# Optimization experiments

Measured on AMD Instinct MI355X. Metric: run time of the kernel, lower is better.

Reference implementation:

```python
import jax, jax.numpy as jnp
import numpy as np
from jax import lax

NK, NV, DK, DV, K, C = 16, 32, 128, 128, 4, 2048
KEY_DIM = NK * DK
VAL_DIM = NV * DV
CONV_DIM = 2 * KEY_DIM + VAL_DIM
EPS = 1e-6


def setup_inputs() -> dict:
    key = jax.random.key(0)
    ks = jax.random.split(key, 10)
    B, T = 2, 2048
    s = 0.02
    return {
        "x": jax.random.normal(ks[0], (B, T, C), jnp.float32),
        "input_pos": jnp.arange(T, dtype=jnp.int32),
        "W_qkv": jax.random.normal(ks[1], (CONV_DIM, C), jnp.float32) * s,
        "W_z": jax.random.normal(ks[2], (VAL_DIM, C), jnp.float32) * s,
        "W_b": jax.random.normal(ks[3], (NV, C), jnp.float32) * s,
        "W_a": jax.random.normal(ks[4], (NV, C), jnp.float32) * s,
        "conv_w": jax.random.normal(ks[5], (CONV_DIM, 1, K), jnp.float32) * 0.1,
        "dt_bias": jnp.ones((NV,), jnp.float32),
        "A_log": jnp.log(jax.random.uniform(ks[6], (NV,), jnp.float32, 1e-3, 16.0)),
        "norm_w": jnp.ones((DV,), jnp.float32),
        "W_out": jax.random.normal(ks[7], (C, VAL_DIM), jnp.float32) * s,
        "conv_state": jnp.zeros((B, CONV_DIM, K), jnp.float32),
        "recurrent_state": jnp.zeros((B, NV, DK, DV), jnp.float32),
    }


def reference(x, input_pos, W_qkv, W_z, W_b, W_a, conv_w, dt_bias, A_log,
              norm_w, W_out, conv_state, recurrent_state):
    B, T, _ = x.shape
    # reset cached state when starting a new sequence (input_pos[0] == 0)
    keep = 1.0 - (input_pos[0] == 0).astype(x.dtype)
    conv_state = conv_state * keep
    state0 = recurrent_state * keep

    qkv = jnp.einsum('btc,dc->btd', x, W_qkv)                      # [B,T,CONV_DIM]
    z = jnp.einsum('btc,dc->btd', x, W_z).reshape(B, T, NV, DV)
    beta = jax.nn.sigmoid(jnp.einsum('btc,hc->bth', x, W_b))       # [B,T,NV]
    a = jnp.einsum('btc,hc->bth', x, W_a)
    g = -jnp.exp(A_log) * jax.nn.softplus(a + dt_bias)             # [B,T,NV]

    # causal depthwise conv using cached conv_state as left context
    conv_in = jnp.concatenate([conv_state, qkv.transpose(0, 2, 1)], axis=-1)  # [B,D,K+T]
    conv_out = lax.conv_general_dilated(
        conv_in, conv_w, (1,), 'VALID',
        dimension_numbers=('NCH', 'OIH', 'NCH'),
        feature_group_count=CONV_DIM)
    qkv_c = jax.nn.silu(conv_out[:, :, -T:]).transpose(0, 2, 1)    # [B,T,CONV_DIM]

    q = qkv_c[..., :KEY_DIM].reshape(B, T, NK, DK)
    k = qkv_c[..., KEY_DIM:2 * KEY_DIM].reshape(B, T, NK, DK)
    v = qkv_c[..., 2 * KEY_DIM:].reshape(B, T, NV, DV)
    q = q / jnp.maximum(jnp.linalg.norm(q, axis=-1, keepdims=True), 1e-12)
    k = k / jnp.maximum(jnp.linalg.norm(k, axis=-1, keepdims=True), 1e-12)
    rep = NV // NK
    if rep > 1:
        q = jnp.repeat(q, rep, axis=2)
        k = jnp.repeat(k, rep, axis=2)

    # gated delta-rule recurrence over time
    def step(carry, xs):
        q_i, k_i, v_i, g_i, b_i = xs                               # [B,H,*]
        new = (jnp.exp(g_i)[..., None, None] * carry
               + b_i[..., None, None] * (k_i[..., :, None] * v_i[..., None, :]))
        out = jnp.einsum('bhk,bhkv->bhv', q_i, new)
        return new, out

    xs = (q.transpose(1, 0, 2, 3), k.transpose(1, 0, 2, 3),
          v.transpose(1, 0, 2, 3), g.transpose(1, 0, 2), beta.transpose(1, 0, 2))
    state, outs = lax.scan(step, state0, xs)
    o = outs.transpose(1, 0, 2, 3)                                 # [B,T,NV,DV]

    # gated RMSNorm (Mamba2-style): gate with silu(z), then RMS-normalize
    o = o * jax.nn.silu(z)
    var = jnp.mean(o * o, axis=-1, keepdims=True)
    o = o * lax.rsqrt(var + EPS) * norm_w
    return jnp.einsum('btd,cd->btc', o.reshape(B, T, VAL_DIM), W_out)
```

## Files before the change

kernel.cpp:

```cpp
#include <hip/hip_runtime.h>
#include <hip/hip_bf16.h>
#include <math.h>

#define NKH 16
#define NVH 32
#define DKD 128
#define DVD 128
#define CDIM 2048
#define KEY_DIM 2048
#define VAL_DIM 4096
#define CONV_DIM 8192
#define BB 2
#define TT 2048
#define MROWS 4096
#define CH 64
#define NCHUNK 32

typedef unsigned short u16;
typedef __bf16 bf16x8 __attribute__((ext_vector_type(8)));
typedef float f32x4 __attribute__((ext_vector_type(4)));

__device__ __forceinline__ u16 f2bf(float f) {
    union { float f; unsigned u; } a; a.f = f;
    unsigned u = a.u;
    u += 0x7fffu + ((u >> 16) & 1u);
    return (u16)(u >> 16);
}
__device__ __forceinline__ float bf2f(u16 h) {
    union { unsigned u; float f; } a; a.u = ((unsigned)h) << 16;
    return a.f;
}
union BF8 { bf16x8 v; uint2 u2[2]; uint4 u4; u16 s[8]; };
__device__ __forceinline__ bf16x8 lds_ld8(const u16* p) {
    BF8 t; t.u2[0] = *(const uint2*)p; t.u2[1] = *(const uint2*)(p + 4); return t.v;
}
__device__ __forceinline__ bf16x8 lds_ld16(const u16* p) {
    BF8 t; t.u4 = *(const uint4*)p; return t.v;
}
__device__ __forceinline__ void lds_st8(u16* p, uint4 v) {
    *(uint2*)p = make_uint2(v.x, v.y); *(uint2*)(p + 4) = make_uint2(v.z, v.w);
}

__global__ __launch_bounds__(256) void fill_kernel(float* __restrict__ p, float v, int n) {
    int i = blockIdx.x * 256 + threadIdx.x;
    if (i < n) p[i] = v;
}

__global__ __launch_bounds__(256) void cast_kernel(const float* __restrict__ src,
                                                   u16* __restrict__ dst, int n4) {
    int i = blockIdx.x * 256 + threadIdx.x;
    if (i >= n4) return;
    float4 v = ((const float4*)src)[i];
    ushort4 r;
    r.x = f2bf(v.x); r.y = f2bf(v.y); r.z = f2bf(v.z); r.w = f2bf(v.w);
    ((ushort4*)dst)[i] = r;
}

template<int OUT_BF16>
__global__ __launch_bounds__(256) void gemm_nt(const u16* __restrict__ A,
                                               const u16* __restrict__ Bm,
                                               void* __restrict__ Cv,
                                               int M, int N, int K) {
    __shared__ __align__(16) u16 As[128 * 64];
    __shared__ __align__(16) u16 Bs[128 * 64];
    const int tid  = threadIdx.x;
    const int lane = tid & 63;
    const int wave = tid >> 6;
    const int m0 = blockIdx.y * 128;
    const int n0 = blockIdx.x * 128;
    const int wm = (wave & 1) * 64;
    const int wn = (wave >> 1) * 64;
    const int l15  = lane & 15;
    const int quad = lane >> 4;

    f32x4 acc[4][4];
#pragma unroll
    for (int i = 0; i < 4; ++i)
#pragma unroll
        for (int j = 0; j < 4; ++j) acc[i][j] = (f32x4)0.0f;

    const int crow = tid >> 3;
    const int ccol = (tid & 7) * 8;

    for (int k0 = 0; k0 < K; k0 += 64) {
#pragma unroll
        for (int p = 0; p < 4; ++p) {
            int row = p * 32 + crow;
            const u16* ga = A + (size_t)(m0 + row) * K + k0 + ccol;
            char* la = (char*)As + (size_t)(p * 256 + (wave << 6)) * 16;
            __builtin_amdgcn_global_load_lds((const __attribute__((address_space(1))) void*)ga,
                                             (__attribute__((address_space(3))) void*)la, 16, 0, 0);
            const u16* gb = Bm + (size_t)(n0 + row) * K + k0 + ccol;
            char* lb = (char*)Bs + (size_t)(p * 256 + (wave << 6)) * 16;
            __builtin_amdgcn_global_load_lds((const __attribute__((address_space(1))) void*)gb,
                                             (__attribute__((address_space(3))) void*)lb, 16, 0, 0);
        }
        __syncthreads();
#pragma unroll
        for (int kk = 0; kk < 64; kk += 32) {
            bf16x8 af[4], bfr[4];
#pragma unroll
            for (int i = 0; i < 4; ++i) {
                af[i]  = *(const bf16x8*)&As[(wm + i * 16 + l15) * 64 + kk + quad * 8];
                bfr[i] = *(const bf16x8*)&Bs[(wn + i * 16 + l15) * 64 + kk + quad * 8];
            }
#pragma unroll
            for (int i = 0; i < 4; ++i)
#pragma unroll
                for (int j = 0; j < 4; ++j)
                    acc[i][j] = __builtin_amdgcn_mfma_f32_16x16x32_bf16(af[i], bfr[j], acc[i][j], 0, 0, 0);
        }
        __syncthreads();
    }
#pragma unroll
    for (int i = 0; i < 4; ++i) {
#pragma unroll
        for (int j = 0; j < 4; ++j) {
#pragma unroll
            for (int r = 0; r < 4; ++r) {
                int grow = m0 + wm + i * 16 + quad * 4 + r;
                int gcol = n0 + wn + j * 16 + l15;
                if (OUT_BF16) {
                    ((u16*)Cv)[(size_t)grow * N + gcol] = f2bf(acc[i][j][r]);
                } else {
                    ((float*)Cv)[(size_t)grow * N + gcol] = acc[i][j][r];
                }
            }
        }
    }
}

template<int OUT_BF16>
__global__ __launch_bounds__(512, 2) void gemm_nt_256(const u16* __restrict__ A,
                                                      const u16* __restrict__ Bm,
                                                      void* __restrict__ Cv,
                                                      int M, int N, int K) {
    __shared__ __align__(16) u16 sA[2][256 * 64];
    __shared__ __align__(16) u16 sB[2][256 * 64];
    const int tid  = threadIdx.x;
    const int lane = tid & 63;
    const int wave = tid >> 6;
    const int wr   = wave >> 2;
    const int wc   = wave & 3;
    const int l15  = lane & 15;
    const int quad = lane >> 4;
    const int m0 = blockIdx.y * 256;
    const int n0 = blockIdx.x * 256;

    f32x4 acc[8][4];
#pragma unroll
    for (int i = 0; i < 8; ++i)
#pragma unroll
        for (int j = 0; j < 4; ++j) acc[i][j] = (f32x4)0.0f;

    auto stage = [&](int buf, int kk0) {
#pragma unroll
        for (int p = 0; p < 4; ++p) {
            const int gbase = p * 512 + wave * 64;
            const int g   = gbase + lane;
            const int row = g >> 3;
            const int sc  = (g & 7) ^ (row & 7);
            const u16* ga = A + (size_t)(m0 + row) * K + kk0 + sc * 8;
            __builtin_amdgcn_global_load_lds(
                (const __attribute__((address_space(1))) void*)ga,
                (__attribute__((address_space(3))) void*)((char*)&sA[buf][0] + (size_t)gbase * 16),
                16, 0, 0);
            const u16* gb = Bm + (size_t)(n0 + row) * K + kk0 + sc * 8;
            __builtin_amdgcn_global_load_lds(
                (const __attribute__((address_space(1))) void*)gb,
                (__attribute__((address_space(3))) void*)((char*)&sB[buf][0] + (size_t)gbase * 16),
                16, 0, 0);
        }
    };

    const int NT = K >> 6;
    stage(0, 0);

    for (int T = 0; T < NT; ++T) {
        const int P = T & 1;
        __builtin_amdgcn_sched_barrier(0);
        if (T + 1 < NT) {
            stage(P ^ 1, (T + 1) << 6);
            asm volatile("s_waitcnt vmcnt(8)" ::: "memory");
        } else {
            asm volatile("s_waitcnt vmcnt(0)" ::: "memory");
        }
        __builtin_amdgcn_s_barrier();
        __builtin_amdgcn_sched_barrier(0);
#pragma unroll
        for (int kk = 0; kk < 2; ++kk) {
            bf16x8 af[8], bfv[4];
#pragma unroll
            for (int i = 0; i < 8; ++i) {
                int row = wr * 128 + i * 16 + l15;
                int slot = ((kk * 4 + quad) ^ (l15 & 7)) * 8;
                af[i] = lds_ld16(&sA[P][row * 64 + slot]);
            }
#pragma unroll
            for (int j = 0; j < 4; ++j) {
                int row = wc * 64 + j * 16 + l15;
                int slot = ((kk * 4 + quad) ^ (l15 & 7)) * 8;
                bfv[j] = lds_ld16(&sB[P][row * 64 + slot]);
            }
#pragma unroll
            for (int i = 0; i < 8; ++i)
#pragma unroll
                for (int j = 0; j < 4; ++j)
                    acc[i][j] = __builtin_amdgcn_mfma_f32_16x16x32_bf16(af[i], bfv[j], acc[i][j], 0, 0, 0);
        }
        __builtin_amdgcn_sched_barrier(0);
        __builtin_amdgcn_s_barrier();
    }

#pragma unroll
    for (int i = 0; i < 8; ++i) {
#pragma unroll
        for (int j = 0; j < 4; ++j) {
#pragma unroll
            for (int r = 0; r < 4; ++r) {
                int grow = m0 + wr * 128 + i * 16 + quad * 4 + r;
                int gcol = n0 + wc * 64 + j * 16 + l15;
                if (OUT_BF16) {
                    ((u16*)Cv)[(size_t)grow * N + gcol] = f2bf(acc[i][j][r]);
                } else {
                    ((float*)Cv)[(size_t)grow * N + gcol] = acc[i][j][r];
                }
            }
        }
    }
}

__global__ __launch_bounds__(256) void bg_epilogue(const float* __restrict__ scores,
                                                   const float* __restrict__ dt_bias,
                                                   const float* __restrict__ A_log,
                                                   float* __restrict__ beta,
                                                   float* __restrict__ g) {
    int i = blockIdx.x * 256 + threadIdx.x;
    int row = i >> 6, col = i & 63;
    float s = scores[(size_t)row * 128 + col];
    if (col < 32) {
        beta[(size_t)row * 32 + col] = 1.f / (1.f + __expf(-s));
    } else {
        int h = col - 32;
        float aa = s + dt_bias[h];
        float sp = (aa > 20.f) ? aa : log1pf(__expf(aa));
        g[(size_t)row * 32 + h] = -__expf(A_log[h]) * sp;
    }
}

__global__ __launch_bounds__(256) void conv_silu_kernel(const u16* __restrict__ qkv,
                                                        const float* __restrict__ conv_w,
                                                        const float* __restrict__ conv_state,
                                                        const int* __restrict__ input_pos,
                                                        u16* __restrict__ qkvc) {
    const int d   = blockIdx.x * 256 + threadIdx.x;
    const int row = blockIdx.y;
    const int t   = row & (TT - 1);
    const int b   = row >> 11;
    const float keep = (input_pos[0] == 0) ? 0.f : 1.f;
    float4 w = *(const float4*)&conv_w[(size_t)d * 4];
    float acc = 0.f;
#pragma unroll
    for (int j = 0; j < 4; ++j) {
        int u = t + j - 3;
        float v;
        if (u >= 0) v = bf2f(qkv[(size_t)(b * TT + u) * CONV_DIM + d]);
        else        v = keep * conv_state[((size_t)b * CONV_DIM + d) * 4 + (u + 4)];
        acc += (&w.x)[j] * v;
    }
    float s = acc / (1.f + __expf(-acc));
    qkvc[(size_t)row * CONV_DIM + d] = f2bf(s);
}

__global__ __launch_bounds__(256) void qknorm_kernel(u16* __restrict__ qkvc) {
    const int gid  = blockIdx.x * 4 + (threadIdx.x >> 6);
    const int lane = threadIdx.x & 63;
    const int row  = gid >> 5;
    const int h    = gid & 31;
    u16* p = qkvc + (size_t)row * CONV_DIM + h * 128;
    ushort2 vb = *(ushort2*)&p[lane * 2];
    float v0 = bf2f(vb.x), v1 = bf2f(vb.y);
    float ss = v0 * v0 + v1 * v1;
#pragma unroll
    for (int off = 32; off; off >>= 1) ss += __shfl_xor(ss, off);
    float scale = 1.f / fmaxf(sqrtf(ss), 1e-12f);
    ushort2 r;
    r.x = f2bf(v0 * scale);
    r.y = f2bf(v1 * scale);
    *(ushort2*)&p[lane * 2] = r;
}

__global__ __launch_bounds__(64) void gates_kernel(const float* __restrict__ g,
                                                   const float* __restrict__ beta_,
                                                   float* __restrict__ gcum,
                                                   float* __restrict__ qsb,
                                                   float* __restrict__ wkb,
                                                   float* __restrict__ dLb) {
    const int bh = blockIdx.x, c = blockIdx.y;
    const int b = bh >> 5, h = bh & 31;
    const int t = threadIdx.x;
    const int row = b * TT + c * CH + t;
    float G = g[(size_t)row * 32 + h];
#pragma unroll
    for (int off = 1; off < 64; off <<= 1) {
        float x = __shfl_up(G, off);
        if (t >= off) G += x;
    }
    float GL = __shfl(G, 63);
    int oidx = bh * TT + c * CH + t;
    gcum[oidx] = G;
    qsb[oidx] = __expf(G);
    wkb[oidx] = __expf(GL - G) * beta_[(size_t)row * 32 + h];
    if (t == 0) dLb[bh * NCHUNK + c] = __expf(GL);
}

__global__ __launch_bounds__(256) void ktrans_kernel(const u16* __restrict__ qkvc,
                                                     u16* __restrict__ kT) {
    const int id = blockIdx.x;
    const int tt = id & 31, dkh = (id >> 5) & 1, hk = (id >> 6) & 15, b = id >> 10;
    const int t0 = tt * 64, dk0 = dkh * 64;
    __shared__ __align__(16) u16 tile[64 * 68];
#pragma unroll
    for (int it = 0; it < 2; ++it) {
        int idx = it * 256 + threadIdx.x;
        int tl = idx >> 3, c8 = (idx & 7) * 8;
        uint4 v = *(const uint4*)&qkvc[(size_t)(b * TT + t0 + tl) * CONV_DIM + KEY_DIM + hk * 128 + dk0 + c8];
        lds_st8(&tile[tl * 68 + c8], v);
    }
    __syncthreads();
#pragma unroll
    for (int it = 0; it < 2; ++it) {
        int idx = it * 256 + threadIdx.x;
        int dkl = idx >> 3, t8 = (idx & 7) * 8;
        unsigned w[4];
#pragma unroll
        for (int p = 0; p < 4; ++p) {
            unsigned lo = tile[(t8 + 2 * p) * 68 + dkl];
            unsigned hi = tile[(t8 + 2 * p + 1) * 68 + dkl];
            w[p] = lo | (hi << 16);
        }
        *(uint4*)&kT[((size_t)((b * 16 + hk) * 128 + dk0 + dkl)) * TT + t0 + t8] =
            make_uint4(w[0], w[1], w[2], w[3]);
    }
}

__global__ __launch_bounds__(256) void chunk_state_kernel(const u16* __restrict__ qkvc,
                                                          const u16* __restrict__ kT,
                                                          const float* __restrict__ qsb,
                                                          const float* __restrict__ wkb,
                                                          const float* __restrict__ dLb,
                                                          const float* __restrict__ rec_state,
                                                          const int* __restrict__ input_pos,
                                                          u16* __restrict__ o) {
    const int b = blockIdx.x, h = blockIdx.y, dvs = blockIdx.z;
    const int tid = threadIdx.x, lane = tid & 63, wave = tid >> 6;
    const int l15 = lane & 15, quad = lane >> 4;
    const int hq = h >> 1, bh = b * 32 + h;
    const float keep = (input_pos[0] == 0) ? 0.f : 1.f;

    __shared__ __align__(16) u16 sQ[64 * 132];
    __shared__ __align__(16) u16 sKT[128 * 68];
    __shared__ __align__(16) u16 sR[32 * 132];
    __shared__ float sQS[64];

    f32x4 st[2][2];
#pragma unroll
    for (int i = 0; i < 2; ++i)
#pragma unroll
        for (int j = 0; j < 2; ++j)
#pragma unroll
            for (int r = 0; r < 4; ++r) {
                int dv = dvs * 32 + i * 16 + quad * 4 + r;
                int dk = wave * 32 + j * 16 + l15;
                st[i][j][r] = keep * rec_state[((size_t)(bh * 128 + dk)) * 128 + dv];
            }

    for (int c = 0; c < NCHUNK; ++c) {
        const int t0 = c * CH;
#pragma unroll
        for (int i = 0; i < 2; ++i)
#pragma unroll
            for (int j = 0; j < 2; ++j)
#pragma unroll
                for (int r = 0; r < 4; ++r)
                    sR[(i * 16 + quad * 4 + r) * 132 + wave * 32 + j * 16 + l15] = f2bf(st[i][j][r]);
#pragma unroll
        for (int it = 0; it < 4; ++it) {
            int idx = it * 256 + tid;
            int t = idx >> 4, c8 = (idx & 15) * 8;
            uint4 v = *(const uint4*)&qkvc[(size_t)(b * TT + t0 + t) * CONV_DIM + hq * 128 + c8];
            lds_st8(&sQ[t * 132 + c8], v);
        }
        if (tid < 64) sQS[tid] = qsb[bh * TT + t0 + tid];
        __syncthreads();
        {
            f32x4 ao[2] = {(f32x4)0.0f, (f32x4)0.0f};
#pragma unroll
            for (int kk = 0; kk < 4; ++kk) {
                bf16x8 af = lds_ld8(&sQ[(wave * 16 + l15) * 132 + kk * 32 + quad * 8]);
                bf16x8 b0 = lds_ld8(&sR[(l15) * 132 + kk * 32 + quad * 8]);
                bf16x8 b1 = lds_ld8(&sR[(16 + l15) * 132 + kk * 32 + quad * 8]);
                ao[0] = __builtin_amdgcn_mfma_f32_16x16x32_bf16(af, b0, ao[0], 0, 0, 0);
                ao[1] = __builtin_amdgcn_mfma_f32_16x16x32_bf16(af, b1, ao[1], 0, 0, 0);
            }
#pragma unroll
            for (int j = 0; j < 2; ++j)
#pragma unroll
                for (int r = 0; r < 4; ++r) {
                    int t = wave * 16 + quad * 4 + r;
                    int dv = dvs * 32 + j * 16 + l15;
                    o[((size_t)(b * TT + t0 + t) * 32 + h) * 128 + dv] = f2bf(ao[j][r] * sQS[t]);
                }
        }
        __syncthreads();
#pragma unroll
        for (int it = 0; it < 4; ++it) {
            int idx = it * 256 + tid;
            int dk = idx >> 3, t8 = (idx & 7) * 8;
            uint4 v = *(const uint4*)&kT[((size_t)((b * 16 + hq) * 128 + dk)) * TT + t0 + t8];
            lds_st8(&sKT[dk * 68 + t8], v);
        }
        {
            int t = tid >> 2, dvo = (tid & 3) * 8;
            float w = wkb[bh * TT + t0 + t];
            BF8 v;
            v.u4 = *(const uint4*)&qkvc[(size_t)(b * TT + t0 + t) * CONV_DIM + 2 * KEY_DIM + h * 128 + dvs * 32 + dvo];
#pragma unroll
            for (int u = 0; u < 8; ++u)
                sR[(dvo + u) * 68 + t] = f2bf(bf2f(v.s[u]) * w);
        }
        __syncthreads();
        {
            float d = dLb[bh * NCHUNK + c];
#pragma unroll
            for (int i = 0; i < 2; ++i)
#pragma unroll
                for (int j = 0; j < 2; ++j)
#pragma unroll
                    for (int r = 0; r < 4; ++r) st[i][j][r] *= d;
#pragma unroll
            for (int kk = 0; kk < 2; ++kk) {
                bf16x8 af[2], bfv[2];
#pragma unroll
                for (int i = 0; i < 2; ++i)
                    af[i] = lds_ld8(&sR[(i * 16 + l15) * 68 + kk * 32 + quad * 8]);
#pragma unroll
                for (int j = 0; j < 2; ++j)
                    bfv[j] = lds_ld8(&sKT[(wave * 32 + j * 16 + l15) * 68 + kk * 32 + quad * 8]);
#pragma unroll
                for (int i = 0; i < 2; ++i)
#pragma unroll
                    for (int j = 0; j < 2; ++j)
                        st[i][j] = __builtin_amdgcn_mfma_f32_16x16x32_bf16(af[i], bfv[j], st[i][j], 0, 0, 0);
            }
        }
        __syncthreads();
    }
}

__global__ __launch_bounds__(256) void chunk_intra_kernel(const u16* __restrict__ qkvc,
                                                          const float* __restrict__ gcum,
                                                          const float* __restrict__ beta_,
                                                          u16* __restrict__ o) {
    const int b = blockIdx.x, h = blockIdx.y, c = blockIdx.z;
    const int tid = threadIdx.x, lane = tid & 63, wave = tid >> 6;
    const int l15 = lane & 15, quad = lane >> 4;
    const int hq = h >> 1, bh = b * 32 + h;
    const int t0 = c * CH;

    __shared__ __align__(16) u16 sQ[64 * 132];
    __shared__ __align__(16) u16 sK[64 * 132];
    __shared__ __align__(16) u16 sVT[128 * 68];
    __shared__ float sG[64];
    __shared__ float sB[64];

#pragma unroll
    for (int it = 0; it < 4; ++it) {
        int idx = it * 256 + tid;
        int t = idx >> 4, c8 = (idx & 15) * 8;
        size_t rbase = (size_t)(b * TT + t0 + t) * CONV_DIM;
        lds_st8(&sQ[t * 132 + c8], *(const uint4*)&qkvc[rbase + hq * 128 + c8]);
        lds_st8(&sK[t * 132 + c8], *(const uint4*)&qkvc[rbase + KEY_DIM + hq * 128 + c8]);
    }
    if (tid < 64) {
        sG[tid] = gcum[bh * TT + t0 + tid];
        sB[tid] = beta_[(size_t)(b * TT + t0 + tid) * 32 + h];
    }
    __syncthreads();
    const int wm = (wave & 1) * 32, wn = (wave >> 1) * 32;
    f32x4 acc[2][2];
#pragma unroll
    for (int i = 0; i < 2; ++i)
#pragma unroll
        for (int j = 0; j < 2; ++j) acc[i][j] = (f32x4)0.0f;
#pragma unroll
    for (int kk = 0; kk < 4; ++kk) {
        bf16x8 af[2], bfv[2];
#pragma unroll
        for (int i = 0; i < 2; ++i) {
            af[i]  = lds_ld8(&sQ[(wm + i * 16 + l15) * 132 + kk * 32 + quad * 8]);
            bfv[i] = lds_ld8(&sK[(wn + i * 16 + l15) * 132 + kk * 32 + quad * 8]);
        }
#pragma unroll
        for (int i = 0; i < 2; ++i)
#pragma unroll
            for (int j = 0; j < 2; ++j)
                acc[i][j] = __builtin_amdgcn_mfma_f32_16x16x32_bf16(af[i], bfv[j], acc[i][j], 0, 0, 0);
    }
    __syncthreads();
#pragma unroll
    for (int i = 0; i < 2; ++i)
#pragma unroll
        for (int j = 0; j < 2; ++j)
#pragma unroll
            for (int r = 0; r < 4; ++r) {
                int t = wm + i * 16 + quad * 4 + r;
                int s = wn + j * 16 + l15;
                float av = 0.f;
                if (s <= t) av = __expf(sG[t] - sG[s]) * sB[s] * acc[i][j][r];
                ((u16*)sQ)[t * 68 + s] = f2bf(av);
            }
#pragma unroll
    for (int it = 0; it < 4; ++it) {
        int idx = it * 256 + tid;
        int t = idx >> 4, c8 = (idx & 15) * 8;
        lds_st8(&sK[t * 132 + c8],
                *(const uint4*)&qkvc[(size_t)(b * TT + t0 + t) * CONV_DIM + 2 * KEY_DIM + h * 128 + c8]);
    }
    __syncthreads();
    {
        int dv = (wave & 1) * 64 + lane;
        int tb = (wave >> 1) * 32;
#pragma unroll
        for (int tc = 0; tc < 4; ++tc) {
            int t8 = tb + tc * 8;
            unsigned w[4];
#pragma unroll
            for (int p = 0; p < 4; ++p) {
                unsigned lo = sK[(t8 + 2 * p) * 132 + dv];
                unsigned hi = sK[(t8 + 2 * p + 1) * 132 + dv];
                w[p] = lo | (hi << 16);
            }
            lds_st8(&sVT[dv * 68 + t8], make_uint4(w[0], w[1], w[2], w[3]));
        }
    }
    __syncthreads();
    const int wm2 = (wave & 1) * 32, wn2 = (wave >> 1) * 64;
    f32x4 oacc[2][4];
#pragma unroll
    for (int i = 0; i < 2; ++i)
#pragma unroll
        for (int j = 0; j < 4; ++j) oacc[i][j] = (f32x4)0.0f;
#pragma unroll
    for (int kk = 0; kk < 2; ++kk) {
        bf16x8 af[2], bfv[4];
#pragma unroll
        for (int i = 0; i < 2; ++i)
            af[i] = lds_ld8(&((u16*)sQ)[(wm2 + i * 16 + l15) * 68 + kk * 32 + quad * 8]);
#pragma unroll
        for (int j = 0; j < 4; ++j)
            bfv[j] = lds_ld8(&sVT[(wn2 + j * 16 + l15) * 68 + kk * 32 + quad * 8]);
#pragma unroll
        for (int i = 0; i < 2; ++i)
#pragma unroll
            for (int j = 0; j < 4; ++j)
                oacc[i][j] = __builtin_amdgcn_mfma_f32_16x16x32_bf16(af[i], bfv[j], oacc[i][j], 0, 0, 0);
    }
#pragma unroll
    for (int i = 0; i < 2; ++i)
#pragma unroll
        for (int j = 0; j < 4; ++j)
#pragma unroll
            for (int r = 0; r < 4; ++r) {
                int t = wm2 + i * 16 + quad * 4 + r;
                int dv = wn2 + j * 16 + l15;
                size_t addr = ((size_t)(b * TT + t0 + t) * 32 + h) * 128 + dv;
                o[addr] = f2bf(oacc[i][j][r] + bf2f(o[addr]));
            }
}

__global__ __launch_bounds__(256) void gnorm_kernel(const u16* __restrict__ o,
                                                    const u16* __restrict__ zb,
                                                    const float* __restrict__ norm_w,
                                                    u16* __restrict__ ob) {
    const int gid  = blockIdx.x * 4 + (threadIdx.x >> 6);
    const int lane = threadIdx.x & 63;
    const int row  = gid >> 5;
    const int h    = gid & 31;
    const size_t base = ((size_t)row * NVH + h) * DVD;
    ushort2 oraw = *(const ushort2*)&o[base + lane * 2];
    float o0 = bf2f(oraw.x), o1 = bf2f(oraw.y);
    float z0 = bf2f(zb[base + lane * 2]);
    float z1 = bf2f(zb[base + lane * 2 + 1]);
    o0 *= z0 / (1.f + __expf(-z0));
    o1 *= z1 / (1.f + __expf(-z1));
    float ss = o0 * o0 + o1 * o1;
#pragma unroll
    for (int off = 32; off; off >>= 1) ss += __shfl_xor(ss, off);
    float scale = rsqrtf(ss * (1.f / 128.f) + 1e-6f);
    float w0 = norm_w[lane * 2], w1 = norm_w[lane * 2 + 1];
    ushort2 r;
    r.x = f2bf(o0 * scale * w0);
    r.y = f2bf(o1 * scale * w1);
    *(ushort2*)&ob[base + lane * 2] = r;
}

extern "C" void kernel_launch(void* const* d_in, const int* in_sizes, int n_in,
                              void* d_out, int out_size, void* d_ws, size_t ws_size,
                              hipStream_t stream) {
    const float* x         = (const float*)d_in[0];
    const int*   input_pos = (const int*)d_in[1];
    const float* W_qkv     = (const float*)d_in[2];
    const float* W_z       = (const float*)d_in[3];
    const float* W_b       = (const float*)d_in[4];
    const float* W_a       = (const float*)d_in[5];
    const float* conv_w    = (const float*)d_in[6];
    const float* dt_bias   = (const float*)d_in[7];
    const float* A_log     = (const float*)d_in[8];
    const float* norm_w    = (const float*)d_in[9];
    const float* W_out     = (const float*)d_in[10];
    const float* conv_state = (const float*)d_in[11];
    const float* rec_state  = (const float*)d_in[12];
    float* out = (float*)d_out;

    const size_t REQUIRED = 168820736;
    if (ws_size < REQUIRED) {
        float mib = (float)((double)ws_size / 1048576.0);
        fill_kernel<<<(out_size + 255) / 256, 256, 0, stream>>>(out, mib, out_size);
        return;
    }

    const size_t MI = 1048576;
    char* ws = (char*)d_ws;
    u16* xb    = (u16*)(ws);
    u16* wqkvb = (u16*)(ws + 16 * MI);
    u16* wzb   = (u16*)(ws + 48 * MI);
    u16* wbab  = (u16*)(ws + 16 * MI);
    float* bgs = (float*)(ws + 17 * MI);
    u16* qkvc  = (u16*)(ws);
    u16* ob    = (u16*)(ws);
    u16* woutb = (u16*)(ws + 32 * MI);
    u16* zb    = (u16*)(ws + 64 * MI);
    u16* qkvb  = (u16*)(ws + 96 * MI);
    u16* o     = (u16*)(ws + 96 * MI);
    u16* kT    = (u16*)(ws + 128 * MI);
    float* gcum = (float*)(ws + 144 * MI);
    float* qsb  = (float*)(ws + 144 * MI + 524288);
    float* wkb  = (float*)(ws + 145 * MI);
    float* dLb  = (float*)(ws + 145 * MI + 524288);
    float* beta = (float*)(ws + 160 * MI);
    float* g    = (float*)(ws + 160 * MI + 524288);

    cast_kernel<<<8192,  256, 0, stream>>>(x,     xb,    2097152);
    cast_kernel<<<16384, 256, 0, stream>>>(W_qkv, wqkvb, 4194304);
    cast_kernel<<<8192,  256, 0, stream>>>(W_z,   wzb,   2097152);

    gemm_nt_256<1><<<dim3(32, 16), 512, 0, stream>>>(xb, wqkvb, qkvb, MROWS, CONV_DIM, CDIM);
    gemm_nt_256<1><<<dim3(16, 16), 512, 0, stream>>>(xb, wzb,   zb,   MROWS, VAL_DIM,  CDIM);

    cast_kernel<<<256, 256, 0, stream>>>(W_b, wbab, 16384);
    cast_kernel<<<256, 256, 0, stream>>>(W_a, wbab + 65536, 16384);
    hipMemsetAsync(wbab + 131072, 0, 131072 * sizeof(u16), stream);
    gemm_nt<0><<<dim3(1, 32), 256, 0, stream>>>(xb, wbab, bgs, MROWS, 128, CDIM);
    bg_epilogue<<<1024, 256, 0, stream>>>(bgs, dt_bias, A_log, beta, g);

    conv_silu_kernel<<<dim3(32, 4096), 256, 0, stream>>>(qkvb, conv_w, conv_state, input_pos, qkvc);
    qknorm_kernel<<<32768, 256, 0, stream>>>(qkvc);

    gates_kernel<<<dim3(64, NCHUNK), 64, 0, stream>>>(g, beta, gcum, qsb, wkb, dLb);
    ktrans_kernel<<<2048, 256, 0, stream>>>(qkvc, kT);
    chunk_state_kernel<<<dim3(BB, NVH, 4), 256, 0, stream>>>(qkvc, kT, qsb, wkb, dLb,
                                                             rec_state, input_pos, o);
    chunk_intra_kernel<<<dim3(BB, NVH, NCHUNK), 256, 0, stream>>>(qkvc, gcum, beta, o);

    cast_kernel<<<8192, 256, 0, stream>>>(W_out, woutb, 2097152);
    gnorm_kernel<<<32768, 256, 0, stream>>>(o, zb, norm_w, ob);

    gemm_nt<0><<<dim3(16, 32), 256, 0, stream>>>(ob, woutb, out, MROWS, CDIM, VAL_DIM);
}
```

Baseline: 777.3 us.

## Interleave A-fragment LDS reads with MFMA quarters in the bf16 GEMM loop

Restructures the GEMM main loop. Each iteration now waits for all outstanding global-to-LDS loads, issues one barrier, and only then starts staging the next K tile. This removes the trailing barrier at the end of the iteration. The B fragments for the tile are loaded up front, while the A fragments are loaded in four quarters, each prefetched while the MFMAs for the previous quarter run. The MFMA blocks are wrapped in s_setprio and separated by barriers between quarters. The aim is to hide LDS read latency behind matrix work and keep more fragments live without holding all eight A fragments at once, at the cost of extra intra-tile barriers and a full vmcnt(0) wait.

```diff
diff --git a/kernel.cpp b/kernel.cpp
--- a/kernel.cpp
+++ b/kernel.cpp
@@ -179,37 +179,61 @@
     for (int T = 0; T < NT; ++T) {
         const int P = T & 1;
         __builtin_amdgcn_sched_barrier(0);
-        if (T + 1 < NT) {
-            stage(P ^ 1, (T + 1) << 6);
-            asm volatile("s_waitcnt vmcnt(8)" ::: "memory");
-        } else {
-            asm volatile("s_waitcnt vmcnt(0)" ::: "memory");
-        }
+        asm volatile("s_waitcnt vmcnt(0)" ::: "memory");
         __builtin_amdgcn_s_barrier();
         __builtin_amdgcn_sched_barrier(0);
-#pragma unroll
-        for (int kk = 0; kk < 2; ++kk) {
-            bf16x8 af[8], bfv[4];
-#pragma unroll
-            for (int i = 0; i < 8; ++i) {
-                int row = wr * 128 + i * 16 + l15;
+        if (T + 1 < NT) stage(P ^ 1, (T + 1) << 6);
+
+        bf16x8 bB[4][2];
+#pragma unroll
+        for (int j = 0; j < 4; ++j)
+#pragma unroll
+            for (int kk = 0; kk < 2; ++kk) {
+                int row  = wc * 64 + j * 16 + l15;
                 int slot = ((kk * 4 + quad) ^ (l15 & 7)) * 8;
-                af[i] = lds_ld16(&sA[P][row * 64 + slot]);
-            }
-#pragma unroll
-            for (int j = 0; j < 4; ++j) {
-                int row = wc * 64 + j * 16 + l15;
+                bB[j][kk] = lds_ld16(&sB[P][row * 64 + slot]);
+            }
+        bf16x8 aC[2][2], aN[2][2];
+#pragma unroll
+        for (int i = 0; i < 2; ++i)
+#pragma unroll
+            for (int kk = 0; kk < 2; ++kk) {
+                int row  = wr * 128 + i * 16 + l15;
                 int slot = ((kk * 4 + quad) ^ (l15 & 7)) * 8;
-                bfv[j] = lds_ld16(&sB[P][row * 64 + slot]);
-            }
-#pragma unroll
-            for (int i = 0; i < 8; ++i)
+                aC[i][kk] = lds_ld16(&sA[P][row * 64 + slot]);
+            }
+
+#pragma unroll
+        for (int q = 0; q < 4; ++q) {
+            if (q < 3) {
+#pragma unroll
+                for (int i = 0; i < 2; ++i)
+#pragma unroll
+                    for (int kk = 0; kk < 2; ++kk) {
+                        int row  = wr * 128 + ((q + 1) * 2 + i) * 16 + l15;
+                        int slot = ((kk * 4 + quad) ^ (l15 & 7)) * 8;
+                        aN[i][kk] = lds_ld16(&sA[P][row * 64 + slot]);
+                    }
+            }
+            __builtin_amdgcn_s_setprio(1);
+#pragma unroll
+            for (int i = 0; i < 2; ++i)
 #pragma unroll
                 for (int j = 0; j < 4; ++j)
-                    acc[i][j] = __builtin_amdgcn_mfma_f32_16x16x32_bf16(af[i], bfv[j], acc[i][j], 0, 0, 0);
-        }
-        __builtin_amdgcn_sched_barrier(0);
-        __builtin_amdgcn_s_barrier();
+#pragma unroll
+                    for (int kk = 0; kk < 2; ++kk)
+                        acc[q * 2 + i][j] = __builtin_amdgcn_mfma_f32_16x16x32_bf16(
+                            aC[i][kk], bB[j][kk], acc[q * 2 + i][j], 0, 0, 0);
+            __builtin_amdgcn_s_setprio(0);
+            __builtin_amdgcn_sched_barrier(0);
+            if (q < 3) {
+                __builtin_amdgcn_s_barrier();
+#pragma unroll
+                for (int i = 0; i < 2; ++i)
+#pragma unroll
+                    for (int kk = 0; kk < 2; ++kk) aC[i][kk] = aN[i][kk];
+            }
+        }
     }
 
 #pragma unroll
```

New measurement: 777.8 us. Within noise of the previous version (+0.1%).

## Deepen GEMM pipeline to 4-stage K=32 buffers, add XCD tile swizzle and LDS swizzle

Applied to the files above, without the earlier changes.

The 256x256 GEMM now uses four LDS buffers of K=32 with three stages in flight and a single barrier per iteration, replacing the two-stage K=64 double buffer. MFMA issue is raised with s_setprio. Both GEMM kernels remap block indices so neighbouring tiles land on the same XCD for L2 reuse. The 128 GEMM also gains an XOR-swizzled LDS layout to cut bank conflicts. The single-barrier scheme depends on the prefetch target buffer not being read by lagging waves, and the smaller K step doubles barrier and waitcnt overhead per unit of K.

```diff
diff --git a/kernel.cpp b/kernel.cpp
--- a/kernel.cpp
+++ b/kernel.cpp
@@ -41,6 +41,25 @@
     *(uint2*)p = make_uint2(v.x, v.y); *(uint2*)(p + 4) = make_uint2(v.z, v.w);
 }
 
+__device__ __forceinline__ void xcd_swizzle(int& tx, int& ty) {
+    const int nx = gridDim.x, ny = gridDim.y;
+    const int b  = blockIdx.x + nx * blockIdx.y;
+    const int nb = nx * ny;
+    if (nx >= 8 && (nx & 7) == 0 && (nb & 255) == 0) {
+        const int rnd  = b >> 8;
+        const int idx  = b & 255;
+        const int xcd  = idx & 7;
+        const int slot = idx >> 3;
+        const int RX   = nx >> 3;
+        const int rx   = xcd & (RX - 1);
+        const int ry   = xcd >> __popc(RX - 1);
+        tx = rx * 8 + (slot & 7);
+        ty = rnd * (256 / nx) + ry * 4 + (slot >> 3);
+    } else {
+        tx = blockIdx.x; ty = blockIdx.y;
+    }
+}
+
 __global__ __launch_bounds__(256) void fill_kernel(float* __restrict__ p, float v, int n) {
     int i = blockIdx.x * 256 + threadIdx.x;
     if (i < n) p[i] = v;
@@ -66,8 +85,10 @@
     const int tid  = threadIdx.x;
     const int lane = tid & 63;
     const int wave = tid >> 6;
-    const int m0 = blockIdx.y * 128;
-    const int n0 = blockIdx.x * 128;
+    int tx, ty;
+    xcd_swizzle(tx, ty);
+    const int m0 = ty * 128;
+    const int n0 = tx * 128;
     const int wm = (wave & 1) * 64;
     const int wn = (wave >> 1) * 64;
     const int l15  = lane & 15;
@@ -80,17 +101,17 @@
         for (int j = 0; j < 4; ++j) acc[i][j] = (f32x4)0.0f;
 
     const int crow = tid >> 3;
-    const int ccol = (tid & 7) * 8;
+    const int scol = ((tid & 7) ^ (crow & 7)) * 8;
 
     for (int k0 = 0; k0 < K; k0 += 64) {
 #pragma unroll
         for (int p = 0; p < 4; ++p) {
             int row = p * 32 + crow;
-            const u16* ga = A + (size_t)(m0 + row) * K + k0 + ccol;
+            const u16* ga = A + (size_t)(m0 + row) * K + k0 + scol;
             char* la = (char*)As + (size_t)(p * 256 + (wave << 6)) * 16;
             __builtin_amdgcn_global_load_lds((const __attribute__((address_space(1))) void*)ga,
                                              (__attribute__((address_space(3))) void*)la, 16, 0, 0);
-            const u16* gb = Bm + (size_t)(n0 + row) * K + k0 + ccol;
+            const u16* gb = Bm + (size_t)(n0 + row) * K + k0 + scol;
             char* lb = (char*)Bs + (size_t)(p * 256 + (wave << 6)) * 16;
             __builtin_amdgcn_global_load_lds((const __attribute__((address_space(1))) void*)gb,
                                              (__attribute__((address_space(3))) void*)lb, 16, 0, 0);
@@ -101,8 +122,9 @@
             bf16x8 af[4], bfr[4];
 #pragma unroll
             for (int i = 0; i < 4; ++i) {
-                af[i]  = *(const bf16x8*)&As[(wm + i * 16 + l15) * 64 + kk + quad * 8];
-                bfr[i] = *(const bf16x8*)&Bs[(wn + i * 16 + l15) * 64 + kk + quad * 8];
+                int sa = (((kk >> 3) + quad) ^ (l15 & 7)) * 8;
+                af[i]  = *(const bf16x8*)&As[(wm + i * 16 + l15) * 64 + sa];
+                bfr[i] = *(const bf16x8*)&Bs[(wn + i * 16 + l15) * 64 + sa];
             }
 #pragma unroll
             for (int i = 0; i < 4; ++i)
@@ -135,8 +157,8 @@
                                                       const u16* __restrict__ Bm,
                                                       void* __restrict__ Cv,
                                                       int M, int N, int K) {
-    __shared__ __align__(16) u16 sA[2][256 * 64];
-    __shared__ __align__(16) u16 sB[2][256 * 64];
+    __shared__ __align__(16) u16 sA[4][256 * 32];
+    __shared__ __align__(16) u16 sB[4][256 * 32];
     const int tid  = threadIdx.x;
     const int lane = tid & 63;
     const int wave = tid >> 6;
@@ -144,8 +166,10 @@
     const int wc   = wave & 3;
     const int l15  = lane & 15;
     const int quad = lane >> 4;
-    const int m0 = blockIdx.y * 256;
-    const int n0 = blockIdx.x * 256;
+    int tx, ty;
+    xcd_swizzle(tx, ty);
+    const int m0 = ty * 256;
+    const int n0 = tx * 256;
 
     f32x4 acc[8][4];
 #pragma unroll
@@ -155,17 +179,17 @@
 
     auto stage = [&](int buf, int kk0) {
 #pragma unroll
-        for (int p = 0; p < 4; ++p) {
+        for (int p = 0; p < 2; ++p) {
             const int gbase = p * 512 + wave * 64;
             const int g   = gbase + lane;
-            const int row = g >> 3;
-            const int sc  = (g & 7) ^ (row & 7);
-            const u16* ga = A + (size_t)(m0 + row) * K + kk0 + sc * 8;
+            const int row = g >> 2;
+            const int sc  = ((g & 3) ^ ((row >> 1) & 3)) * 8;
+            const u16* ga = A + (size_t)(m0 + row) * K + kk0 + sc;
             __builtin_amdgcn_global_load_lds(
                 (const __attribute__((address_space(1))) void*)ga,
                 (__attribute__((address_space(3))) void*)((char*)&sA[buf][0] + (size_t)gbase * 16),
                 16, 0, 0);
-            const u16* gb = Bm + (size_t)(n0 + row) * K + kk0 + sc * 8;
+            const u16* gb = Bm + (size_t)(n0 + row) * K + kk0 + sc;
             __builtin_amdgcn_global_load_lds(
                 (const __attribute__((address_space(1))) void*)gb,
                 (__attribute__((address_space(3))) void*)((char*)&sB[buf][0] + (size_t)gbase * 16),
@@ -173,43 +197,41 @@
         }
     };
 
-    const int NT = K >> 6;
+    const int NT = K >> 5;
     stage(0, 0);
+    stage(1, 32);
+    stage(2, 64);
+
+    const int slot8 = (quad ^ ((l15 >> 1) & 3)) * 8;
 
     for (int T = 0; T < NT; ++T) {
-        const int P = T & 1;
+        const int P = T & 3;
         __builtin_amdgcn_sched_barrier(0);
-        if (T + 1 < NT) {
-            stage(P ^ 1, (T + 1) << 6);
-            asm volatile("s_waitcnt vmcnt(8)" ::: "memory");
-        } else {
-            asm volatile("s_waitcnt vmcnt(0)" ::: "memory");
-        }
+        if (T + 2 < NT)      asm volatile("s_waitcnt vmcnt(8)" ::: "memory");
+        else if (T + 1 < NT) asm volatile("s_waitcnt vmcnt(4)" ::: "memory");
+        else                 asm volatile("s_waitcnt vmcnt(0)" ::: "memory");
         __builtin_amdgcn_s_barrier();
         __builtin_amdgcn_sched_barrier(0);
-#pragma unroll
-        for (int kk = 0; kk < 2; ++kk) {
-            bf16x8 af[8], bfv[4];
-#pragma unroll
-            for (int i = 0; i < 8; ++i) {
-                int row = wr * 128 + i * 16 + l15;
-                int slot = ((kk * 4 + quad) ^ (l15 & 7)) * 8;
-                af[i] = lds_ld16(&sA[P][row * 64 + slot]);
-            }
-#pragma unroll
-            for (int j = 0; j < 4; ++j) {
-                int row = wc * 64 + j * 16 + l15;
-                int slot = ((kk * 4 + quad) ^ (l15 & 7)) * 8;
-                bfv[j] = lds_ld16(&sB[P][row * 64 + slot]);
-            }
-#pragma unroll
-            for (int i = 0; i < 8; ++i)
-#pragma unroll
-                for (int j = 0; j < 4; ++j)
-                    acc[i][j] = __builtin_amdgcn_mfma_f32_16x16x32_bf16(af[i], bfv[j], acc[i][j], 0, 0, 0);
-        }
-        __builtin_amdgcn_sched_barrier(0);
-        __builtin_amdgcn_s_barrier();
+        if (T + 3 < NT) stage((T + 3) & 3, (T + 3) << 5);
+
+        bf16x8 aF[8], bF[4];
+#pragma unroll
+        for (int j = 0; j < 4; ++j) {
+            int row = wc * 64 + j * 16 + l15;
+            bF[j] = lds_ld16(&sB[P][row * 32 + slot8]);
+        }
+#pragma unroll
+        for (int i = 0; i < 8; ++i) {
+            int row = wr * 128 + i * 16 + l15;
+            aF[i] = lds_ld16(&sA[P][row * 32 + slot8]);
+        }
+        __builtin_amdgcn_s_setprio(1);
+#pragma unroll
+        for (int i = 0; i < 8; ++i)
+#pragma unroll
+            for (int j = 0; j < 4; ++j)
+                acc[i][j] = __builtin_amdgcn_mfma_f32_16x16x32_bf16(aF[i], bF[j], acc[i][j], 0, 0, 0);
+        __builtin_amdgcn_s_setprio(0);
     }
 
 #pragma unroll
```

Measured after the change: 794.1 us. 2.2% more time.
